# Optimization experiments

Hardware: AMD Instinct MI355X
Metric: run time of the kernel (lower is better)

Reference implementation:

```python
import jax, jax.numpy as jnp
import numpy as np

S, N, H = 4096, 32, 512

def setup_inputs() -> dict:
    key = jax.random.key(0)
    ks = jax.random.split(key, 8)
    scale = 1.0 / np.sqrt(H)
    return {
        "hidden": jax.random.normal(ks[0], (N, H), dtype=jnp.float32),
        "encoder_outputs": jax.random.normal(ks[1], (S, N, H), dtype=jnp.float32),
        "W_w": jax.random.uniform(ks[2], (H, H), jnp.float32, -scale, scale),
        "W_b": jax.random.uniform(ks[3], (H,), jnp.float32, -scale, scale),
        "U_w": jax.random.uniform(ks[4], (H, H), jnp.float32, -scale, scale),
        "U_b": jax.random.uniform(ks[5], (H,), jnp.float32, -scale, scale),
        "v_w": jax.random.uniform(ks[6], (1, H), jnp.float32, -scale, scale),
        "v_b": jax.random.uniform(ks[7], (1,), jnp.float32, -scale, scale),
    }

def reference(hidden, encoder_outputs, W_w, W_b, U_w, U_b, v_w, v_b):
    # W(hidden): [N,H] -> broadcast over seq dim (equivalent to expand then Linear)
    wh = hidden @ W_w.T + W_b                      # [N, H]
    ue = jnp.einsum('snh,kh->snk', encoder_outputs, U_w) + U_b  # [S, N, H]
    energy = jnp.tanh(wh[None, :, :] + ue)         # [S, N, H]
    score = jnp.einsum('snh,oh->sno', energy, v_w) + v_b        # [S, N, 1]
    attention_weights = jax.nn.softmax(score, axis=0)           # softmax over seq
    context = jnp.sum(attention_weights * encoder_outputs, axis=0)  # [N, H]
    return (context, attention_weights)
```

## Files before the change

### kernel.cpp

```cpp
#include <hip/hip_runtime.h>
#include <hip/hip_bf16.h>

#define Sdim 4096
#define Ndim 32
#define Hdim 512
#define Mdim (Sdim * Ndim)

#define BM 128
#define BN 256
#define BK 64

typedef __bf16 bf16x8 __attribute__((ext_vector_type(8)));
typedef float f32x4 __attribute__((ext_vector_type(4)));
typedef unsigned short ushort8v __attribute__((ext_vector_type(8)));

__device__ __forceinline__ void load_lds16(const void* g, void* l) {
    __builtin_amdgcn_global_load_lds(
        (const __attribute__((address_space(1))) void*)g,
        (__attribute__((address_space(3))) void*)l, 16, 0, 0);
}

__device__ __forceinline__ float ftanh(float x) {
    float e = __expf(2.f * x);
    return 1.f - 2.f / (e + 1.f);
}

__global__ __launch_bounds__(256) void k_prep_bias(
    const float* __restrict__ hidden, const float* __restrict__ Ww,
    const float* __restrict__ Wb, const float* __restrict__ Ubias,
    float* __restrict__ bias) {
    const int t = threadIdx.x, w = t >> 6, lane = t & 63;
    const int cc = blockIdx.x * 4 + w;
    const float4 w0 = *(const float4*)(Ww + (size_t)cc * Hdim + lane * 8);
    const float4 w1 = *(const float4*)(Ww + (size_t)cc * Hdim + lane * 8 + 4);
    const float wb = Wb[cc] + Ubias[cc];
    for (int n = 0; n < Ndim; ++n) {
        const float4 h0 = *(const float4*)(hidden + n * Hdim + lane * 8);
        const float4 h1 = *(const float4*)(hidden + n * Hdim + lane * 8 + 4);
        float p = w0.x * h0.x + w0.y * h0.y + w0.z * h0.z + w0.w * h0.w +
                  w1.x * h1.x + w1.y * h1.y + w1.z * h1.z + w1.w * h1.w;
        p += __shfl_xor(p, 1);  p += __shfl_xor(p, 2);
        p += __shfl_xor(p, 4);  p += __shfl_xor(p, 8);
        p += __shfl_xor(p, 16); p += __shfl_xor(p, 32);
        if (lane == 0) bias[n * Hdim + cc] = p + wb;
    }
}

__global__ __launch_bounds__(256) void k_cvt(
    const float* __restrict__ src, unsigned short* __restrict__ dst) {
    const int i = blockIdx.x * 256 + threadIdx.x;
    float4 v = ((const float4*)src)[i];
    union { __hip_bfloat162 h[2]; ushort4 u; } r;
    r.h[0] = __float22bfloat162_rn(make_float2(v.x, v.y));
    r.h[1] = __float22bfloat162_rn(make_float2(v.z, v.w));
    ((ushort4*)dst)[i] = r.u;
}

__global__ __launch_bounds__(512, 4) void k_gemm_score(
    const float* __restrict__ enc,
    const unsigned short* __restrict__ Ub,
    const float* __restrict__ bias,
    const float* __restrict__ vw,
    float* __restrict__ scorep) {
    __shared__ __align__(16) unsigned short Asm[BM][72];
    __shared__ __align__(16) unsigned short Bsm[BN * BK];
    __shared__ float ssm[4][BM];

    const int t = threadIdx.x;
    const int lane = t & 63;
    const int w = t >> 6;
    const int wM = w >> 2;
    const int wN = w & 3;
    const int c = lane & 15;
    const int q = lane >> 4;

    const int rowblk = blockIdx.x >> 1;
    const int colblk = blockIdx.x & 1;
    const int mBase = rowblk * BM;
    const int colBase = colblk * BN;

    const int ar = t >> 2;
    const int aq = t & 3;
    const int asw = ((ar >> 3) & 1) << 1;
    const float4* arow =
        (const float4*)(enc + (size_t)(mBase + ar) * Hdim) + aq * 4;
    unsigned short* awr = &Asm[ar][((2 * aq) ^ asw) * 8];

    const int coff = lane >> 3;
    const int bch = (lane & 7) ^ coff;
    const unsigned short* bsrc =
        Ub + (size_t)(colBase + w * 8 + coff) * Hdim + bch * 8;
    unsigned short* bdst = Bsm + (w * 8) * BK;

    const int sA = ((c >> 3) & 1) << 1;
    const int sB = c & 7;

    f32x4 acc[4][4];
#pragma unroll
    for (int i = 0; i < 4; ++i)
#pragma unroll
        for (int j = 0; j < 4; ++j) acc[i][j] = (f32x4){0.f, 0.f, 0.f, 0.f};

    float4 a0 = arow[0], a1 = arow[1], a2 = arow[2], a3 = arow[3];

#pragma unroll 1
    for (int kk = 0; kk < Hdim / BK; ++kk) {
        asm volatile("" ::: "memory");
        __builtin_amdgcn_s_barrier();
        asm volatile("" ::: "memory");
        __builtin_amdgcn_sched_barrier(0);

#pragma unroll
        for (int g = 0; g < 4; ++g)
            load_lds16(bsrc + (size_t)g * 64 * Hdim + kk * BK,
                       bdst + g * 64 * BK);
        asm volatile("" ::: "memory");
        __builtin_amdgcn_sched_barrier(0);

        union { __hip_bfloat162 h[4]; ushort8v v; } p0, p1;
        p0.h[0] = __float22bfloat162_rn(make_float2(a0.x, a0.y));
        p0.h[1] = __float22bfloat162_rn(make_float2(a0.z, a0.w));
        p0.h[2] = __float22bfloat162_rn(make_float2(a1.x, a1.y));
        p0.h[3] = __float22bfloat162_rn(make_float2(a1.z, a1.w));
        p1.h[0] = __float22bfloat162_rn(make_float2(a2.x, a2.y));
        p1.h[1] = __float22bfloat162_rn(make_float2(a2.z, a2.w));
        p1.h[2] = __float22bfloat162_rn(make_float2(a3.x, a3.y));
        p1.h[3] = __float22bfloat162_rn(make_float2(a3.z, a3.w));
        *(ushort8v*)awr = p0.v;
        *(ushort8v*)(awr + 8) = p1.v;

        const int kn = (kk < Hdim / BK - 1) ? kk + 1 : kk;
        const float4* ap = arow + kn * 16;
        a0 = ap[0]; a1 = ap[1]; a2 = ap[2]; a3 = ap[3];

        asm volatile("" ::: "memory");
        __builtin_amdgcn_sched_barrier(0);
        asm volatile("s_waitcnt vmcnt(4) lgkmcnt(0)" ::: "memory");
        __builtin_amdgcn_s_barrier();
        asm volatile("" ::: "memory");
        __builtin_amdgcn_sched_barrier(0);

#pragma unroll 1
        for (int h = 0; h < 2; ++h) {
            bf16x8 af[4], bfr[4];
#pragma unroll
            for (int mi = 0; mi < 4; ++mi) {
                const int row = wM * 64 + mi * 16 + c;
                af[mi] =
                    *(const bf16x8*)&Asm[row][(((h << 2) | q) ^ sA) * 8];
            }
#pragma unroll
            for (int ni = 0; ni < 4; ++ni) {
                const int lc = wN * 64 + ni * 16 + c;
                bfr[ni] = *(const bf16x8*)&Bsm[lc * BK +
                                               (((h << 2) | q) ^ sB) * 8];
            }
#pragma unroll
            for (int mi = 0; mi < 4; ++mi)
#pragma unroll
                for (int ni = 0; ni < 4; ++ni)
                    acc[mi][ni] = __builtin_amdgcn_mfma_f32_16x16x32_bf16(
                        af[mi], bfr[ni], acc[mi][ni], 0, 0, 0);
        }
    }
    asm volatile("" :: "v"(a0.x), "v"(a1.x), "v"(a2.x), "v"(a3.x));

    float vcol[4];
#pragma unroll
    for (int ni = 0; ni < 4; ++ni)
        vcol[ni] = vw[colBase + wN * 64 + ni * 16 + c];

#pragma unroll
    for (int mi = 0; mi < 4; ++mi) {
#pragma unroll
        for (int reg = 0; reg < 4; ++reg) {
            const int rl = wM * 64 + mi * 16 + q * 4 + reg;
            const int n = rl & 31;
            float p = 0.f;
#pragma unroll
            for (int ni = 0; ni < 4; ++ni) {
                const int col = colBase + wN * 64 + ni * 16 + c;
                float e = acc[mi][ni][reg] + bias[n * Hdim + col];
                p += vcol[ni] * ftanh(e);
            }
            p += __shfl_xor(p, 1);
            p += __shfl_xor(p, 2);
            p += __shfl_xor(p, 4);
            p += __shfl_xor(p, 8);
            if (c == 0) ssm[wN][rl] = p;
        }
    }
    __syncthreads();
    if (t < BM) {
        const int m = mBase + t;
        const float s = ssm[0][t] + ssm[1][t] + ssm[2][t] + ssm[3][t];
        scorep[colblk * Mdim + (m & 31) * Sdim + (m >> 5)] = s;
    }
}

__global__ __launch_bounds__(256) void k_softmax(
    const float* __restrict__ scorep,
    float* __restrict__ out_w) {
    const int n = blockIdx.x;
    const int t = threadIdx.x;
    const int w = t >> 6;
    __shared__ float row[Sdim];
    __shared__ float red[8];
    const float4* s0 = (const float4*)(scorep + n * Sdim);
    const float4* s1 = (const float4*)(scorep + Mdim + n * Sdim);

    float mx = -1e30f;
    for (int i = t; i < Sdim / 4; i += 256) {
        float4 a = s0[i], b = s1[i];
        float4 v;
        v.x = a.x + b.x; v.y = a.y + b.y; v.z = a.z + b.z; v.w = a.w + b.w;
        ((float4*)row)[i] = v;
        mx = fmaxf(mx, fmaxf(fmaxf(v.x, v.y), fmaxf(v.z, v.w)));
    }
#pragma unroll
    for (int o = 32; o > 0; o >>= 1) mx = fmaxf(mx, __shfl_xor(mx, o));
    if ((t & 63) == 0) red[w] = mx;
    __syncthreads();
    mx = fmaxf(fmaxf(red[0], red[1]), fmaxf(red[2], red[3]));

    float sum = 0.f;
    for (int i = t; i < Sdim; i += 256) sum += __expf(row[i] - mx);
#pragma unroll
    for (int o = 32; o > 0; o >>= 1) sum += __shfl_xor(sum, o);
    if ((t & 63) == 0) red[4 + w] = sum;
    __syncthreads();
    sum = red[4] + red[5] + red[6] + red[7];
    const float inv = 1.f / sum;
    for (int i = t; i < Sdim; i += 256)
        out_w[i * Ndim + n] = __expf(row[i] - mx) * inv;
}

__global__ __launch_bounds__(512) void k_context(
    const float* __restrict__ enc, const float* __restrict__ wts,
    float* __restrict__ part) {
    const int n = blockIdx.x & 31;
    const int sc = blockIdx.x >> 5;
    const int s0 = sc * 256;
    const int t = threadIdx.x;
    const int g = t >> 6;
    const int lane = t & 63;
    const int h0 = lane * 8;
    float4 c0 = {0.f, 0.f, 0.f, 0.f}, c1 = {0.f, 0.f, 0.f, 0.f};
#pragma unroll 4
    for (int it = 0; it < 32; ++it) {
        const int s = s0 + it * 8 + g;
        const float wv = wts[(size_t)s * Ndim + n];
        const float* e = enc + ((size_t)s * Ndim + n) * Hdim + h0;
        const float4 e0 = *(const float4*)e;
        const float4 e1 = *(const float4*)(e + 4);
        c0.x += wv * e0.x; c0.y += wv * e0.y;
        c0.z += wv * e0.z; c0.w += wv * e0.w;
        c1.x += wv * e1.x; c1.y += wv * e1.y;
        c1.z += wv * e1.z; c1.w += wv * e1.w;
    }
    __shared__ __align__(16) float4 red[7][128];
    if (g > 0) { red[g - 1][lane * 2] = c0; red[g - 1][lane * 2 + 1] = c1; }
    __syncthreads();
    if (g == 0) {
#pragma unroll
        for (int i = 0; i < 7; ++i) {
            const float4 b0 = red[i][lane * 2];
            const float4 b1 = red[i][lane * 2 + 1];
            c0.x += b0.x; c0.y += b0.y; c0.z += b0.z; c0.w += b0.w;
            c1.x += b1.x; c1.y += b1.y; c1.z += b1.z; c1.w += b1.w;
        }
        float* o = part + (size_t)(sc * 32 + n) * Hdim + h0;
        *(float4*)o = c0;
        *(float4*)(o + 4) = c1;
    }
}

__global__ __launch_bounds__(256) void k_ctx_reduce(
    const float* __restrict__ part, float* __restrict__ out) {
    const int j = blockIdx.x * 256 + threadIdx.x;
    float4 s = {0.f, 0.f, 0.f, 0.f};
    for (int i = 0; i < 16; ++i) {
        const float4 v = ((const float4*)part)[i * 4096 + j];
        s.x += v.x; s.y += v.y; s.z += v.z; s.w += v.w;
    }
    ((float4*)out)[j] = s;
}

extern "C" void kernel_launch(void* const* d_in, const int* in_sizes, int n_in,
                              void* d_out, int out_size, void* d_ws,
                              size_t ws_size, hipStream_t stream) {
    const float* hidden = (const float*)d_in[0];
    const float* enc    = (const float*)d_in[1];
    const float* Ww     = (const float*)d_in[2];
    const float* Wb     = (const float*)d_in[3];
    const float* Uw     = (const float*)d_in[4];
    const float* Ubias  = (const float*)d_in[5];
    const float* vw     = (const float*)d_in[6];

    float* out = (float*)d_out;

    char* ws = (char*)d_ws;
    float* bias          = (float*)(ws);
    unsigned short* Ub16 = (unsigned short*)(ws + (64 << 10));
    float* scorep        = (float*)(ws + (576 << 10));
    float* part          = (float*)(ws + (64 << 10));

    k_prep_bias<<<128, 256, 0, stream>>>(hidden, Ww, Wb, Ubias, bias);
    k_cvt<<<256, 256, 0, stream>>>(Uw, Ub16);
    k_gemm_score<<<(Mdim / BM) * 2, 512, 0, stream>>>(enc, Ub16, bias, vw,
                                                      scorep);
    k_softmax<<<Ndim, 256, 0, stream>>>(scorep, out + Ndim * Hdim);
    k_context<<<Ndim * (Sdim / 256), 512, 0, stream>>>(enc, out + Ndim * Hdim,
                                                       part);
    k_ctx_reduce<<<16, 256, 0, stream>>>(part, out);
}
```

Baseline: 483.1 us.

## Double-buffer GEMM with BK=32, remap block order, fuse softmax into context

The score GEMM moves to BK=32 with double-buffered A and B shared-memory tiles, so loads for the next K step overlap the MFMAs of the current one. The XOR swizzle is dropped and the block index is remapped so neighbouring blocks share a column tile. Softmax is split into a small kernel that only computes the exp-sum, and the context kernel now computes the normalised weights itself, writes them out, and uses twice as many S chunks. The max subtraction is removed, so exp overflow is possible for large scores, and the unswizzled LDS layout may cause bank conflicts.

```diff
diff --git a/kernel.cpp b/kernel.cpp
--- a/kernel.cpp
+++ b/kernel.cpp
@@ -8,7 +8,8 @@
 
 #define BM 128
 #define BN 256
-#define BK 64
+#define BK 32
+#define NKS (Hdim / BK)
 
 typedef __bf16 bf16x8 __attribute__((ext_vector_type(8)));
 typedef float f32x4 __attribute__((ext_vector_type(4)));
@@ -62,8 +63,8 @@
     const float* __restrict__ bias,
     const float* __restrict__ vw,
     float* __restrict__ scorep) {
-    __shared__ __align__(16) unsigned short Asm[BM][72];
-    __shared__ __align__(16) unsigned short Bsm[BN * BK];
+    __shared__ __align__(16) unsigned short Asm[2][BM * BK];
+    __shared__ __align__(16) unsigned short Bsm[2][BN * BK];
     __shared__ float ssm[4][BM];
 
     const int t = threadIdx.x;
@@ -74,26 +75,22 @@
     const int c = lane & 15;
     const int q = lane >> 4;
 
-    const int rowblk = blockIdx.x >> 1;
-    const int colblk = blockIdx.x & 1;
+    const int x = blockIdx.x;
+    const int rowblk = (x & 7) | ((x >> 4) << 3);
+    const int colblk = (x >> 3) & 1;
     const int mBase = rowblk * BM;
     const int colBase = colblk * BN;
 
-    const int ar = t >> 2;
-    const int aq = t & 3;
-    const int asw = ((ar >> 3) & 1) << 1;
-    const float4* arow =
-        (const float4*)(enc + (size_t)(mBase + ar) * Hdim) + aq * 4;
-    unsigned short* awr = &Asm[ar][((2 * aq) ^ asw) * 8];
-
-    const int coff = lane >> 3;
-    const int bch = (lane & 7) ^ coff;
-    const unsigned short* bsrc =
-        Ub + (size_t)(colBase + w * 8 + coff) * Hdim + bch * 8;
-    unsigned short* bdst = Bsm + (w * 8) * BK;
-
-    const int sA = ((c >> 3) & 1) << 1;
-    const int sB = c & 7;
+    const float* asrc = enc + (size_t)(mBase + (t >> 2)) * Hdim + (t & 3) * 8;
+    unsigned short* const adst0 = &Asm[0][t * 8];
+    unsigned short* const adst1 = &Asm[1][t * 8];
+
+    const int u0 = (w << 7) + lane;
+    const int u1 = u0 + 64;
+    const unsigned short* bsrc0 =
+        Ub + (size_t)(colBase + (u0 >> 2)) * Hdim + (u0 & 3) * 8;
+    const unsigned short* bsrc1 =
+        Ub + (size_t)(colBase + (u1 >> 2)) * Hdim + (u1 & 3) * 8;
 
     f32x4 acc[4][4];
 #pragma unroll
@@ -101,69 +98,70 @@
 #pragma unroll
         for (int j = 0; j < 4; ++j) acc[i][j] = (f32x4){0.f, 0.f, 0.f, 0.f};
 
-    float4 a0 = arow[0], a1 = arow[1], a2 = arow[2], a3 = arow[3];
+    float4 pa0 = *(const float4*)(asrc);
+    float4 pa1 = *(const float4*)(asrc + 4);
+    load_lds16(bsrc0, &Bsm[0][w * 1024]);
+    load_lds16(bsrc1, &Bsm[0][w * 1024 + 512]);
+    asm volatile("" ::: "memory");
+    __builtin_amdgcn_sched_barrier(0);
+    {
+        union { __hip_bfloat162 h[4]; ushort8v v; } pk;
+        pk.h[0] = __float22bfloat162_rn(make_float2(pa0.x, pa0.y));
+        pk.h[1] = __float22bfloat162_rn(make_float2(pa0.z, pa0.w));
+        pk.h[2] = __float22bfloat162_rn(make_float2(pa1.x, pa1.y));
+        pk.h[3] = __float22bfloat162_rn(make_float2(pa1.z, pa1.w));
+        *(ushort8v*)adst0 = pk.v;
+    }
+    pa0 = *(const float4*)(asrc + BK);
+    pa1 = *(const float4*)(asrc + BK + 4);
+    asm volatile("" ::: "memory");
+    __builtin_amdgcn_sched_barrier(0);
+    asm volatile("s_waitcnt vmcnt(2) lgkmcnt(0)" ::: "memory");
+    __builtin_amdgcn_s_barrier();
+    __builtin_amdgcn_sched_barrier(0);
 
 #pragma unroll 1
-    for (int kk = 0; kk < Hdim / BK; ++kk) {
-        asm volatile("" ::: "memory");
-        __builtin_amdgcn_s_barrier();
+    for (int kk = 0; kk < NKS; ++kk) {
+        const int cur = kk & 1, nxt = cur ^ 1;
+        const int kb = (kk + 1 < NKS) ? kk + 1 : NKS - 1;
+        load_lds16(bsrc0 + kb * BK, &Bsm[nxt][w * 1024]);
+        load_lds16(bsrc1 + kb * BK, &Bsm[nxt][w * 1024 + 512]);
         asm volatile("" ::: "memory");
         __builtin_amdgcn_sched_barrier(0);
-
-#pragma unroll
-        for (int g = 0; g < 4; ++g)
-            load_lds16(bsrc + (size_t)g * 64 * Hdim + kk * BK,
-                       bdst + g * 64 * BK);
+        {
+            union { __hip_bfloat162 h[4]; ushort8v v; } pk;
+            pk.h[0] = __float22bfloat162_rn(make_float2(pa0.x, pa0.y));
+            pk.h[1] = __float22bfloat162_rn(make_float2(pa0.z, pa0.w));
+            pk.h[2] = __float22bfloat162_rn(make_float2(pa1.x, pa1.y));
+            pk.h[3] = __float22bfloat162_rn(make_float2(pa1.z, pa1.w));
+            *(ushort8v*)(nxt ? adst1 : adst0) = pk.v;
+        }
+        const int ka = (kk + 2 < NKS) ? kk + 2 : NKS - 1;
+        pa0 = *(const float4*)(asrc + ka * BK);
+        pa1 = *(const float4*)(asrc + ka * BK + 4);
         asm volatile("" ::: "memory");
         __builtin_amdgcn_sched_barrier(0);
-
-        union { __hip_bfloat162 h[4]; ushort8v v; } p0, p1;
-        p0.h[0] = __float22bfloat162_rn(make_float2(a0.x, a0.y));
-        p0.h[1] = __float22bfloat162_rn(make_float2(a0.z, a0.w));
-        p0.h[2] = __float22bfloat162_rn(make_float2(a1.x, a1.y));
-        p0.h[3] = __float22bfloat162_rn(make_float2(a1.z, a1.w));
-        p1.h[0] = __float22bfloat162_rn(make_float2(a2.x, a2.y));
-        p1.h[1] = __float22bfloat162_rn(make_float2(a2.z, a2.w));
-        p1.h[2] = __float22bfloat162_rn(make_float2(a3.x, a3.y));
-        p1.h[3] = __float22bfloat162_rn(make_float2(a3.z, a3.w));
-        *(ushort8v*)awr = p0.v;
-        *(ushort8v*)(awr + 8) = p1.v;
-
-        const int kn = (kk < Hdim / BK - 1) ? kk + 1 : kk;
-        const float4* ap = arow + kn * 16;
-        a0 = ap[0]; a1 = ap[1]; a2 = ap[2]; a3 = ap[3];
-
-        asm volatile("" ::: "memory");
+        bf16x8 af[4], bfr[4];
+#pragma unroll
+        for (int mi = 0; mi < 4; ++mi)
+            af[mi] = *(const bf16x8*)&Asm[cur][(wM * 64 + mi * 16 + c) * BK +
+                                              q * 8];
+#pragma unroll
+        for (int ni = 0; ni < 4; ++ni)
+            bfr[ni] = *(const bf16x8*)&Bsm[cur][(wN * 64 + ni * 16 + c) * BK +
+                                               q * 8];
+#pragma unroll
+        for (int mi = 0; mi < 4; ++mi)
+#pragma unroll
+            for (int ni = 0; ni < 4; ++ni)
+                acc[mi][ni] = __builtin_amdgcn_mfma_f32_16x16x32_bf16(
+                    af[mi], bfr[ni], acc[mi][ni], 0, 0, 0);
+        asm volatile("s_waitcnt vmcnt(2) lgkmcnt(0)" ::: "memory");
         __builtin_amdgcn_sched_barrier(0);
-        asm volatile("s_waitcnt vmcnt(4) lgkmcnt(0)" ::: "memory");
         __builtin_amdgcn_s_barrier();
-        asm volatile("" ::: "memory");
         __builtin_amdgcn_sched_barrier(0);
-
-#pragma unroll 1
-        for (int h = 0; h < 2; ++h) {
-            bf16x8 af[4], bfr[4];
-#pragma unroll
-            for (int mi = 0; mi < 4; ++mi) {
-                const int row = wM * 64 + mi * 16 + c;
-                af[mi] =
-                    *(const bf16x8*)&Asm[row][(((h << 2) | q) ^ sA) * 8];
-            }
-#pragma unroll
-            for (int ni = 0; ni < 4; ++ni) {
-                const int lc = wN * 64 + ni * 16 + c;
-                bfr[ni] = *(const bf16x8*)&Bsm[lc * BK +
-                                               (((h << 2) | q) ^ sB) * 8];
-            }
-#pragma unroll
-            for (int mi = 0; mi < 4; ++mi)
-#pragma unroll
-                for (int ni = 0; ni < 4; ++ni)
-                    acc[mi][ni] = __builtin_amdgcn_mfma_f32_16x16x32_bf16(
-                        af[mi], bfr[ni], acc[mi][ni], 0, 0, 0);
-        }
-    }
-    asm volatile("" :: "v"(a0.x), "v"(a1.x), "v"(a2.x), "v"(a3.x));
+    }
+    asm volatile("" :: "v"(pa0.x), "v"(pa1.x));
 
     float vcol[4];
 #pragma unroll
@@ -198,58 +196,55 @@
     }
 }
 
-__global__ __launch_bounds__(256) void k_softmax(
+__global__ __launch_bounds__(256) void k_sumexp(
     const float* __restrict__ scorep,
-    float* __restrict__ out_w) {
+    float* __restrict__ sums) {
     const int n = blockIdx.x;
     const int t = threadIdx.x;
     const int w = t >> 6;
-    __shared__ float row[Sdim];
-    __shared__ float red[8];
-    const float4* s0 = (const float4*)(scorep + n * Sdim);
-    const float4* s1 = (const float4*)(scorep + Mdim + n * Sdim);
-
-    float mx = -1e30f;
+    const float4* p0 = (const float4*)(scorep + n * Sdim);
+    const float4* p1 = (const float4*)(scorep + Mdim + n * Sdim);
+    float s = 0.f;
     for (int i = t; i < Sdim / 4; i += 256) {
-        float4 a = s0[i], b = s1[i];
-        float4 v;
-        v.x = a.x + b.x; v.y = a.y + b.y; v.z = a.z + b.z; v.w = a.w + b.w;
-        ((float4*)row)[i] = v;
-        mx = fmaxf(mx, fmaxf(fmaxf(v.x, v.y), fmaxf(v.z, v.w)));
-    }
-#pragma unroll
-    for (int o = 32; o > 0; o >>= 1) mx = fmaxf(mx, __shfl_xor(mx, o));
-    if ((t & 63) == 0) red[w] = mx;
+        const float4 a = p0[i], b = p1[i];
+        s += __expf(a.x + b.x) + __expf(a.y + b.y) + __expf(a.z + b.z) +
+             __expf(a.w + b.w);
+    }
+#pragma unroll
+    for (int o = 32; o > 0; o >>= 1) s += __shfl_xor(s, o);
+    __shared__ float red[4];
+    if ((t & 63) == 0) red[w] = s;
     __syncthreads();
-    mx = fmaxf(fmaxf(red[0], red[1]), fmaxf(red[2], red[3]));
-
-    float sum = 0.f;
-    for (int i = t; i < Sdim; i += 256) sum += __expf(row[i] - mx);
-#pragma unroll
-    for (int o = 32; o > 0; o >>= 1) sum += __shfl_xor(sum, o);
-    if ((t & 63) == 0) red[4 + w] = sum;
-    __syncthreads();
-    sum = red[4] + red[5] + red[6] + red[7];
-    const float inv = 1.f / sum;
-    for (int i = t; i < Sdim; i += 256)
-        out_w[i * Ndim + n] = __expf(row[i] - mx) * inv;
+    if (t == 0) sums[n] = 1.f / (red[0] + red[1] + red[2] + red[3]);
 }
 
 __global__ __launch_bounds__(512) void k_context(
-    const float* __restrict__ enc, const float* __restrict__ wts,
+    const float* __restrict__ enc, const float* __restrict__ scorep,
+    const float* __restrict__ sums, float* __restrict__ out_w,
     float* __restrict__ part) {
     const int n = blockIdx.x & 31;
     const int sc = blockIdx.x >> 5;
-    const int s0 = sc * 256;
+    const int s0 = sc * 128;
     const int t = threadIdx.x;
     const int g = t >> 6;
     const int lane = t & 63;
     const int h0 = lane * 8;
+
+    __shared__ float wsm[128];
+    if (t < 128) {
+        const int s = s0 + t;
+        const float sv = scorep[n * Sdim + s] + scorep[Mdim + n * Sdim + s];
+        const float wv = __expf(sv) * sums[n];
+        wsm[t] = wv;
+        out_w[(size_t)s * Ndim + n] = wv;
+    }
+    __syncthreads();
+
     float4 c0 = {0.f, 0.f, 0.f, 0.f}, c1 = {0.f, 0.f, 0.f, 0.f};
 #pragma unroll 4
-    for (int it = 0; it < 32; ++it) {
+    for (int it = 0; it < 16; ++it) {
         const int s = s0 + it * 8 + g;
-        const float wv = wts[(size_t)s * Ndim + n];
+        const float wv = wsm[it * 8 + g];
         const float* e = enc + ((size_t)s * Ndim + n) * Hdim + h0;
         const float4 e0 = *(const float4*)e;
         const float4 e1 = *(const float4*)(e + 4);
@@ -279,7 +274,7 @@
     const float* __restrict__ part, float* __restrict__ out) {
     const int j = blockIdx.x * 256 + threadIdx.x;
     float4 s = {0.f, 0.f, 0.f, 0.f};
-    for (int i = 0; i < 16; ++i) {
+    for (int i = 0; i < 32; ++i) {
         const float4 v = ((const float4*)part)[i * 4096 + j];
         s.x += v.x; s.y += v.y; s.z += v.z; s.w += v.w;
     }
@@ -303,14 +298,15 @@
     float* bias          = (float*)(ws);
     unsigned short* Ub16 = (unsigned short*)(ws + (64 << 10));
     float* scorep        = (float*)(ws + (576 << 10));
-    float* part          = (float*)(ws + (64 << 10));
+    float* sums          = (float*)(ws + (1600 << 10));
+    float* part          = (float*)(ws + (1664 << 10));
 
     k_prep_bias<<<128, 256, 0, stream>>>(hidden, Ww, Wb, Ubias, bias);
     k_cvt<<<256, 256, 0, stream>>>(Uw, Ub16);
     k_gemm_score<<<(Mdim / BM) * 2, 512, 0, stream>>>(enc, Ub16, bias, vw,
                                                       scorep);
-    k_softmax<<<Ndim, 256, 0, stream>>>(scorep, out + Ndim * Hdim);
-    k_context<<<Ndim * (Sdim / 256), 512, 0, stream>>>(enc, out + Ndim * Hdim,
-                                                       part);
+    k_sumexp<<<Ndim, 256, 0, stream>>>(scorep, sums);
+    k_context<<<Ndim * (Sdim / 128), 512, 0, stream>>>(enc, scorep, sums,
+                                                       out + Ndim * Hdim, part);
     k_ctx_reduce<<<16, 256, 0, stream>>>(part, out);
 }
```

After: 526.5 us. 1.09x slower.
